# Kernel optimization log

Measured on AMD Instinct MI355X. Metric: run time of the kernel, lower is better.

## Reference

```python
import jax, jax.numpy as jnp
import numpy as np

B, S, H, NH = 4, 2048, 1024, 16
DK = H // NH


def setup_inputs() -> dict:
    key = jax.random.key(0)
    ks = jax.random.split(key, 12)
    sd = 1.0 / np.sqrt(H)
    inp = {
        "query": jax.random.normal(ks[0], (B, S, H), jnp.float32),
        "key_": jax.random.normal(ks[1], (B, S, H), jnp.float32),
        "value": jax.random.normal(ks[2], (B, S, H), jnp.float32),
        "mask": jax.random.randint(ks[3], (B, 1, S, S), 0, 2) == 1,
        "Wq": jax.random.uniform(ks[4], (H, H), jnp.float32, -sd, sd),
        "bq": jnp.zeros((H,), jnp.float32),
        "Wk": jax.random.uniform(ks[5], (H, H), jnp.float32, -sd, sd),
        "bk": jnp.zeros((H,), jnp.float32),
        "Wv": jax.random.uniform(ks[6], (H, H), jnp.float32, -sd, sd),
        "bv": jnp.zeros((H,), jnp.float32),
        "Wo": jax.random.uniform(ks[7], (H, H), jnp.float32, -sd, sd),
        "bo": jnp.zeros((H,), jnp.float32),
    }
    return inp


def reference(query, key_, value, mask, Wq, bq, Wk, bk, Wv, bv, Wo, bo):
    b = query.shape[0]
    # projections; nn.Linear computes x @ W^T + b
    q = (query @ Wq.T + bq).reshape(b, -1, NH, DK).transpose(0, 2, 1, 3)  # [B,NH,S,DK]
    k = (key_ @ Wk.T + bk).reshape(b, -1, NH, DK).transpose(0, 2, 1, 3)
    v = (value @ Wv.T + bv).reshape(b, -1, NH, DK).transpose(0, 2, 1, 3)
    scores = jnp.einsum("bhqd,bhkd->bhqk", q, k) / jnp.sqrt(jnp.float32(DK))
    min_val = jnp.finfo(scores.dtype).min
    scores = jnp.where(mask, min_val, scores)
    attn = jax.nn.softmax(scores, axis=-1)
    attn = jnp.where(mask, 0.0, attn)
    # dropout_rate = 0.0 -> identity
    x = jnp.einsum("bhqk,bhkd->bhqd", attn, v)
    x = x.transpose(0, 2, 1, 3).reshape(b, -1, NH * DK)  # [B,S,H]
    return x @ Wo.T + bo
```

## Files before the change

### kernel.cpp

```cpp
#include <hip/hip_runtime.h>
#include <hip/hip_bf16.h>
#include <stdint.h>

#define B_  4
#define S_  2048
#define H_  1024
#define NH_ 16
#define DK_ 64
#define M_  (B_*S_)

typedef unsigned short u16;
typedef __attribute__((ext_vector_type(8))) short bfrag;
typedef __attribute__((ext_vector_type(4))) float facc;
typedef __attribute__((ext_vector_type(16))) float f32x16;
typedef __attribute__((ext_vector_type(4))) unsigned int u32x4;
typedef __attribute__((ext_vector_type(2))) unsigned int u32x2;

__device__ __forceinline__ u16 f2bf(float f) {
  uint32_t u = __float_as_uint(f);
  return (u16)((u + 0x7fffu + ((u >> 16) & 1u)) >> 16);
}

__device__ __forceinline__ uint32_t cvtpk_bf16(float a, float b) {
  uint32_t r;
  asm("v_cvt_pk_bf16_f32 %0, %1, %2" : "=v"(r) : "v"(a), "v"(b));
  return r;
}

__device__ __forceinline__ f32x16 zero16() {
  f32x16 z;
  #pragma unroll
  for (int e = 0; e < 16; e++) z[e] = 0.f;
  return z;
}

__global__ void cvt3_kernel(const float* __restrict__ a0, const float* __restrict__ a1,
                            const float* __restrict__ a2,
                            u16* __restrict__ o0, u16* __restrict__ o1, u16* __restrict__ o2,
                            int n4) {
  const float* in = blockIdx.y == 0 ? a0 : blockIdx.y == 1 ? a1 : a2;
  u16* out = blockIdx.y == 0 ? o0 : blockIdx.y == 1 ? o1 : o2;
  int i = blockIdx.x * blockDim.x + threadIdx.x;
  int stride = gridDim.x * blockDim.x;
  for (; i < n4; i += stride) {
    float4 v = reinterpret_cast<const float4*>(in)[i];
    ushort4 o;
    o.x = f2bf(v.x); o.y = f2bf(v.y); o.z = f2bf(v.z); o.w = f2bf(v.w);
    reinterpret_cast<ushort4*>(out)[i] = o;
  }
}

__global__ void cvt4_kernel(const float* __restrict__ a0, const float* __restrict__ a1,
                            const float* __restrict__ a2, const float* __restrict__ a3,
                            u16* __restrict__ o0, u16* __restrict__ o1,
                            u16* __restrict__ o2, u16* __restrict__ o3,
                            int n4, float s0) {
  int y = blockIdx.y;
  const float* in = y == 0 ? a0 : y == 1 ? a1 : y == 2 ? a2 : a3;
  u16* out = y == 0 ? o0 : y == 1 ? o1 : y == 2 ? o2 : o3;
  float sc = (y == 0) ? s0 : 1.0f;
  int i = blockIdx.x * blockDim.x + threadIdx.x;
  int stride = gridDim.x * blockDim.x;
  for (; i < n4; i += stride) {
    float4 v = reinterpret_cast<const float4*>(in)[i];
    ushort4 o;
    o.x = f2bf(v.x * sc); o.y = f2bf(v.y * sc);
    o.z = f2bf(v.z * sc); o.w = f2bf(v.w * sc);
    reinterpret_cast<ushort4*>(out)[i] = o;
  }
}

__global__ void pack_mask_kernel(const int* __restrict__ m, uint32_t* __restrict__ bits, int nwords) {
  int w = blockIdx.x * blockDim.x + threadIdx.x;
  if (w >= nwords) return;
  const int4* p = reinterpret_cast<const int4*>(m) + (size_t)w * 8;
  uint32_t word = 0;
  #pragma unroll
  for (int i = 0; i < 8; i++) {
    int4 v = p[i];
    word |= (uint32_t)(v.x != 0) << (i*4);
    word |= (uint32_t)(v.y != 0) << (i*4+1);
    word |= (uint32_t)(v.z != 0) << (i*4+2);
    word |= (uint32_t)(v.w != 0) << (i*4+3);
  }
  bits[w] = word;
}

#define GLD16(gsrc, ldst) \
  __builtin_amdgcn_global_load_lds((const __attribute__((address_space(1))) void*)(gsrc), \
                                   (__attribute__((address_space(3))) void*)(ldst), 16, 0, 0)

__global__ __launch_bounds__(256) void qkv_gemm(const u16* __restrict__ qa, const u16* __restrict__ ka,
                                                const u16* __restrict__ va,
                                                const u16* __restrict__ Wqb, const u16* __restrict__ Wkb,
                                                const u16* __restrict__ Wvb,
                                                const float* __restrict__ bqp, const float* __restrict__ bkp,
                                                const float* __restrict__ bvp, float qbscale,
                                                u16* __restrict__ qh, u16* __restrict__ kh,
                                                u16* __restrict__ vt) {
  constexpr int K = H_;
  __shared__ __align__(16) u16 As[128*32];
  __shared__ __align__(16) u16 Bs[128*32];
  const int tid = threadIdx.x;
  const int lane = tid & 63, wave = tid >> 6;
  const int lo = lane & 15, hi = lane >> 4;
  const int wr = wave >> 1, wc = wave & 1;
  const int wsel = blockIdx.y >> 3;
  const int m0 = blockIdx.x * 128, n0 = (blockIdx.y & 7) * 128;
  const u16* A  = wsel == 0 ? qa : wsel == 1 ? ka : va;
  const u16* Bm = wsel == 0 ? Wqb : wsel == 1 ? Wkb : Wvb;
  const float* bias = wsel == 0 ? bqp : wsel == 1 ? bkp : bvp;
  const float bscale = wsel == 0 ? qbscale : 1.0f;
  facc acc[4][4] = {};

  for (int k0 = 0; k0 < K; k0 += 32) {
    const u16* Ab = A + (size_t)m0 * K + k0;
    const u16* Bb = Bm + (size_t)n0 * K + k0;
    #pragma unroll
    for (int i = 0; i < 2; i++) {
      int idx = i*256 + tid;
      int row = idx >> 2, q = idx & 3;
      char* la = (char*)As + i*4096 + wave*1024;
      char* lb = (char*)Bs + i*4096 + wave*1024;
      GLD16(Ab + (size_t)row*K + q*8, la);
      GLD16(Bb + (size_t)row*K + q*8, lb);
    }
    __syncthreads();
    bfrag af[4], bfv[4];
    #pragma unroll
    for (int t = 0; t < 4; t++) {
      af[t]  = *reinterpret_cast<const bfrag*>(&As[(wr*64 + t*16 + lo)*32 + hi*8]);
      bfv[t] = *reinterpret_cast<const bfrag*>(&Bs[(wc*64 + t*16 + lo)*32 + hi*8]);
    }
    #pragma unroll
    for (int mt = 0; mt < 4; mt++)
      #pragma unroll
      for (int nt = 0; nt < 4; nt++)
        acc[mt][nt] = __builtin_amdgcn_mfma_f32_16x16x32_bf16(af[mt], bfv[nt], acc[mt][nt], 0, 0, 0);
    __syncthreads();
  }

  if (wsel < 2) {
    u16* o = wsel == 0 ? qh : kh;
    #pragma unroll
    for (int nt = 0; nt < 4; nt++) {
      int n = n0 + wc*64 + nt*16 + lo;
      float bv = bias[n] * bscale;
      int hh = n >> 6, d = n & 63;
      #pragma unroll
      for (int mt = 0; mt < 4; mt++) {
        #pragma unroll
        for (int r = 0; r < 4; r++) {
          int m = m0 + wr*64 + mt*16 + hi*4 + r;
          int bb = m >> 11, s = m & (S_ - 1);
          o[(((size_t)bb*NH_ + hh)*S_ + s)*DK_ + d] = f2bf(acc[mt][nt][r] + bv);
        }
      }
    }
  } else {
    #pragma unroll
    for (int nt = 0; nt < 4; nt++) {
      int n = n0 + wc*64 + nt*16 + lo;
      float bv = bias[n];
      int hh = n >> 6, d = n & 63;
      #pragma unroll
      for (int mt = 0; mt < 4; mt++) {
        #pragma unroll
        for (int r = 0; r < 4; r++) {
          int m = m0 + wr*64 + mt*16 + hi*4 + r;
          int bb = m >> 11, s = m & (S_ - 1);
          vt[(((size_t)bb*NH_ + hh)*DK_ + d)*S_ + s] = f2bf(acc[mt][nt][r] + bv);
        }
      }
    }
  }
}

__global__ __launch_bounds__(256) void gemm_out(const u16* __restrict__ A, const u16* __restrict__ Bm,
                                                const float* __restrict__ bias, float* __restrict__ o) {
  constexpr int K = H_, N = H_;
  __shared__ __align__(16) u16 As[128*32];
  __shared__ __align__(16) u16 Bs[128*32];
  const int tid = threadIdx.x;
  const int lane = tid & 63, wave = tid >> 6;
  const int lo = lane & 15, hi = lane >> 4;
  const int wr = wave >> 1, wc = wave & 1;
  const int m0 = blockIdx.x * 128, n0 = blockIdx.y * 128;
  facc acc[4][4] = {};

  for (int k0 = 0; k0 < K; k0 += 32) {
    const u16* Ab = A + (size_t)m0 * K + k0;
    const u16* Bb = Bm + (size_t)n0 * K + k0;
    #pragma unroll
    for (int i = 0; i < 2; i++) {
      int idx = i*256 + tid;
      int row = idx >> 2, q = idx & 3;
      char* la = (char*)As + i*4096 + wave*1024;
      char* lb = (char*)Bs + i*4096 + wave*1024;
      GLD16(Ab + (size_t)row*K + q*8, la);
      GLD16(Bb + (size_t)row*K + q*8, lb);
    }
    __syncthreads();
    bfrag af[4], bfv[4];
    #pragma unroll
    for (int t = 0; t < 4; t++) {
      af[t]  = *reinterpret_cast<const bfrag*>(&As[(wr*64 + t*16 + lo)*32 + hi*8]);
      bfv[t] = *reinterpret_cast<const bfrag*>(&Bs[(wc*64 + t*16 + lo)*32 + hi*8]);
    }
    #pragma unroll
    for (int mt = 0; mt < 4; mt++)
      #pragma unroll
      for (int nt = 0; nt < 4; nt++)
        acc[mt][nt] = __builtin_amdgcn_mfma_f32_16x16x32_bf16(af[mt], bfv[nt], acc[mt][nt], 0, 0, 0);
    __syncthreads();
  }

  #pragma unroll
  for (int nt = 0; nt < 4; nt++) {
    int n = n0 + wc*64 + nt*16 + lo;
    float bv = bias[n];
    #pragma unroll
    for (int mt = 0; mt < 4; mt++) {
      #pragma unroll
      for (int r = 0; r < 4; r++) {
        int m = m0 + wr*64 + mt*16 + hi*4 + r;
        o[(size_t)m*N + n] = acc[mt][nt][r] + bv;
      }
    }
  }
}

__global__ __launch_bounds__(256, 4) void attn_kernel(const u16* __restrict__ Qh, const u16* __restrict__ Kh,
                                                      const u16* __restrict__ Vt, const uint32_t* __restrict__ mbits,
                                                      u16* __restrict__ xout) {
  __shared__ __align__(16) u16 Ks[2][64*64];
  __shared__ __align__(16) u16 Vs[2][64*64];
  const int tid = threadIdx.x;
  const int lane = tid & 63, wave = tid >> 6;
  const int l31 = lane & 31, hl = lane >> 5;
  const int gid = blockIdx.x;
  const int bh = (gid & 7) * 8 + (gid >> 7);
  const int qt = (gid >> 3) & 15;
  const int b = bh >> 4, hd = bh & 15;
  const int q0 = qt * 128;
  const size_t bhS = (size_t)bh * S_;
  const int swz = (lane & 7) << 4;

  bfrag qf[4];
  {
    const u16* qrow = Qh + (bhS + q0 + wave*32 + l31) * DK_;
    #pragma unroll
    for (int t = 0; t < 4; t++) qf[t] = *reinterpret_cast<const bfrag*>(qrow + t*16 + hl*8);
  }
  const uint32_t* mrow = mbits + ((size_t)b * S_ + q0 + wave*32 + l31) * 64;

  const int srow = wave*8 + (lane >> 3);
  const int scol = ((lane & 7) ^ (lane >> 3)) * 16;
  const char* ksrc = (const char*)(Kh + bhS * DK_) + (size_t)srow * 128 + scol;
  const char* vsrc = (const char*)(Vt + (size_t)bh * DK_ * S_) + (size_t)srow * (S_*2) + scol;

#define STAGE(buf, c) { \
    char* kl = (char*)Ks[buf] + wave*1024; \
    char* vl = (char*)Vs[buf] + wave*1024; \
    GLD16(ksrc + (size_t)(c)*8192,          kl); \
    GLD16(ksrc + (size_t)(c)*8192 + 4096,   kl + 4096); \
    GLD16(vsrc + (size_t)(c)*128,           vl); \
    GLD16(vsrc + (size_t)(c)*128 + 131072,  vl + 4096); \
  }

  float m_run = -1e29f, l_run = 0.f;
  f32x16 accO[2];
  accO[0] = zero16(); accO[1] = zero16();

  STAGE(0, 0);
  __syncthreads();

  for (int c = 0; c < 32; c++) {
    const int cur = c & 1;
    if (c + 1 < 32) STAGE(cur ^ 1, c + 1);

    const char* KsB = (const char*)Ks[cur];
    f32x16 s0 = zero16(), s1 = zero16();
    __builtin_amdgcn_s_setprio(1);
    #pragma unroll
    for (int t = 0; t < 4; t++) {
      bfrag k0 = *reinterpret_cast<const bfrag*>(KsB + l31*128        + ((t*32 + hl*16) ^ swz));
      bfrag k1 = *reinterpret_cast<const bfrag*>(KsB + (32 + l31)*128 + ((t*32 + hl*16) ^ swz));
      s0 = __builtin_amdgcn_mfma_f32_32x32x16_bf16(k0, qf[t], s0, 0, 0, 0);
      s1 = __builtin_amdgcn_mfma_f32_32x32x16_bf16(k1, qf[t], s1, 0, 0, 0);
    }
    __builtin_amdgcn_s_setprio(0);

    uint2 mwv = *reinterpret_cast<const uint2*>(mrow + c*2);
    uint32_t w0 = mwv.x >> (4*hl), w1 = mwv.y >> (4*hl);
    float sv0[16], sv1[16];
    #pragma unroll
    for (int r = 0; r < 16; r++) {
      int sh = (r & 3) + 8*(r >> 2);
      sv0[r] = ((w0 >> sh) & 1u) ? -1e30f : s0[r];
      sv1[r] = ((w1 >> sh) & 1u) ? -1e30f : s1[r];
    }
    float mc = -1e30f;
    #pragma unroll
    for (int r = 0; r < 16; r++) mc = fmaxf(mc, fmaxf(sv0[r], sv1[r]));
    mc = fmaxf(mc, __shfl_xor(mc, 32));
    if (!__all(mc <= m_run + 8.f)) {
      float mnew = fmaxf(m_run, mc);
      float alpha = __builtin_amdgcn_exp2f(m_run - mnew);
      m_run = mnew;
      l_run *= alpha;
      accO[0] = accO[0] * alpha;
      accO[1] = accO[1] * alpha;
    }
    #pragma unroll
    for (int r = 0; r < 16; r++) {
      sv0[r] = __builtin_amdgcn_exp2f(sv0[r] - m_run);
      sv1[r] = __builtin_amdgcn_exp2f(sv1[r] - m_run);
    }
    float lsum = 0.f;
    #pragma unroll
    for (int r = 0; r < 16; r++) lsum += sv0[r] + sv1[r];
    lsum += __shfl_xor(lsum, 32);
    l_run += lsum;

    u32x4 pa[4];
    #pragma unroll
    for (int kt = 0; kt < 2; kt++) {
      uint32_t W[8];
      #pragma unroll
      for (int j = 0; j < 8; j++)
        W[j] = kt == 0 ? cvtpk_bf16(sv0[2*j], sv0[2*j+1]) : cvtpk_bf16(sv1[2*j], sv1[2*j+1]);
      u32x2 r02 = __builtin_amdgcn_permlane32_swap(W[0], W[2], false, false);
      u32x2 r13 = __builtin_amdgcn_permlane32_swap(W[1], W[3], false, false);
      u32x2 r46 = __builtin_amdgcn_permlane32_swap(W[4], W[6], false, false);
      u32x2 r57 = __builtin_amdgcn_permlane32_swap(W[5], W[7], false, false);
      pa[kt*2    ][0] = r02.x; pa[kt*2    ][1] = r13.x; pa[kt*2    ][2] = r02.y; pa[kt*2    ][3] = r13.y;
      pa[kt*2 + 1][0] = r46.x; pa[kt*2 + 1][1] = r57.x; pa[kt*2 + 1][2] = r46.y; pa[kt*2 + 1][3] = r57.y;
    }

    const char* VsB = (const char*)Vs[cur];
    __builtin_amdgcn_s_setprio(1);
    #pragma unroll
    for (int ks = 0; ks < 4; ks++) {
      bfrag pb = __builtin_bit_cast(bfrag, pa[ks]);
      bfrag v0 = *reinterpret_cast<const bfrag*>(VsB + l31*128        + ((ks*32 + hl*16) ^ swz));
      bfrag v1 = *reinterpret_cast<const bfrag*>(VsB + (32 + l31)*128 + ((ks*32 + hl*16) ^ swz));
      accO[0] = __builtin_amdgcn_mfma_f32_32x32x16_bf16(v0, pb, accO[0], 0, 0, 0);
      accO[1] = __builtin_amdgcn_mfma_f32_32x32x16_bf16(v1, pb, accO[1], 0, 0, 0);
    }
    __builtin_amdgcn_s_setprio(0);
    __syncthreads();
  }
#undef STAGE

  float linv = (l_run > 0.f) ? (1.f / l_run) : 0.f;
  u16* Xs = (u16*)Ks;
  {
    char* xb = (char*)Xs + (wave*32 + l31) * 128;
    #pragma unroll
    for (int dt = 0; dt < 2; dt++)
      #pragma unroll
      for (int j = 0; j < 8; j++) {
        uint32_t w = cvtpk_bf16(accO[dt][2*j] * linv, accO[dt][2*j+1] * linv);
        int d = dt*32 + ((2*j) & 3) + 8*((2*j) >> 2) + 4*hl;
        *reinterpret_cast<uint32_t*>(xb + ((d*2) ^ swz)) = w;
      }
  }
  __syncthreads();
  {
    int row = tid >> 1, d0 = (tid & 1) * 32;
    int rsw = (row & 7) << 4;
    u16* orow = xout + ((size_t)b * S_ + q0 + row) * H_ + hd * DK_ + d0;
    #pragma unroll
    for (int i = 0; i < 4; i++) {
      bfrag v = *reinterpret_cast<const bfrag*>((char*)Xs + row*128 + ((d0*2 + i*16) ^ rsw));
      *reinterpret_cast<bfrag*>((char*)orow + i*16) = v;
    }
  }
}

extern "C" void kernel_launch(void* const* d_in, const int* in_sizes, int n_in,
                              void* d_out, int out_size, void* d_ws, size_t ws_size,
                              hipStream_t stream) {
  const float* query = (const float*)d_in[0];
  const float* key_  = (const float*)d_in[1];
  const float* value = (const float*)d_in[2];
  const int*   mask  = (const int*)d_in[3];
  const float* Wq = (const float*)d_in[4];
  const float* bq = (const float*)d_in[5];
  const float* Wk = (const float*)d_in[6];
  const float* bk = (const float*)d_in[7];
  const float* Wv = (const float*)d_in[8];
  const float* bv = (const float*)d_in[9];
  const float* Wo = (const float*)d_in[10];
  const float* bo = (const float*)d_in[11];
  float* out = (float*)d_out;

  char* ws = (char*)d_ws;
  const size_t MB = 1024 * 1024;
  u16* q_act = (u16*)(ws + 0*MB);
  u16* k_act = (u16*)(ws + 16*MB);
  u16* v_act = (u16*)(ws + 32*MB);
  u16* wq_b  = (u16*)(ws + 48*MB);
  u16* wk_b  = (u16*)(ws + 50*MB);
  u16* wv_b  = (u16*)(ws + 52*MB);
  u16* wo_b  = (u16*)(ws + 54*MB);
  u16* qh    = (u16*)(ws + 56*MB);
  u16* kh    = (u16*)(ws + 72*MB);
  u16* vt    = (u16*)(ws + 104*MB);
  u16* xb    = (u16*)(ws + 120*MB);
  uint32_t* mbits = (uint32_t*)(ws + 136*MB);

  const float QSCALE = 0.125f * 1.44269504088896f;

  const int nact4 = M_ * H_ / 4;
  cvt3_kernel<<<dim3(1024, 3), 256, 0, stream>>>(query, key_, value, q_act, k_act, v_act, nact4);
  const int nw4 = H_ * H_ / 4;
  cvt4_kernel<<<dim3(256, 4), 256, 0, stream>>>(Wq, Wk, Wv, Wo, wq_b, wk_b, wv_b, wo_b, nw4, QSCALE);
  const int nwords = B_ * S_ * S_ / 32;
  pack_mask_kernel<<<nwords/256, 256, 0, stream>>>(mask, mbits, nwords);

  qkv_gemm<<<dim3(M_/128, 24), 256, 0, stream>>>(q_act, k_act, v_act, wq_b, wk_b, wv_b,
                                                 bq, bk, bv, QSCALE, qh, kh, vt);
  attn_kernel<<<1024, 256, 0, stream>>>(qh, kh, vt, mbits, xb);
  gemm_out<<<dim3(M_/128, H_/128), 256, 0, stream>>>(xb, wo_b, bo, out);
}
```

Before: 264.4 us.

## Fold mask into MFMA accumulator init and defer row-sum shuffle to epilogue

The mask bits are now applied by seeding the QK^T MFMA accumulators with -1e30 or 0 instead of selecting after the matmul, and the mask word for the next chunk is prefetched one iteration ahead. Max and sum reductions are rewritten as balanced trees to shorten dependency chains. The cross-half shuffle for the softmax denominator moves out of the loop into the epilogue. This trims VALU work and latency in the softmax section of the attention loop. Masked scores now come from adding the dot product to -1e30, which still gives zero weight after exp.

```diff
diff --git a/kernel.cpp b/kernel.cpp
--- a/kernel.cpp
+++ b/kernel.cpp
@@ -273,14 +273,26 @@
   accO[0] = zero16(); accO[1] = zero16();
 
   STAGE(0, 0);
+  uint2 mw_cur = *reinterpret_cast<const uint2*>(mrow);
   __syncthreads();
 
   for (int c = 0; c < 32; c++) {
     const int cur = c & 1;
     if (c + 1 < 32) STAGE(cur ^ 1, c + 1);
 
+    uint2 mw = mw_cur;
+    if (c + 1 < 32) mw_cur = *reinterpret_cast<const uint2*>(mrow + (c + 1)*2);
+
+    uint32_t w0 = mw.x >> (4*hl), w1 = mw.y >> (4*hl);
+    f32x16 s0, s1;
+    #pragma unroll
+    for (int r = 0; r < 16; r++) {
+      const int sh = (r & 3) + 8*(r >> 2);
+      s0[r] = ((w0 >> sh) & 1u) ? -1e30f : 0.0f;
+      s1[r] = ((w1 >> sh) & 1u) ? -1e30f : 0.0f;
+    }
+
     const char* KsB = (const char*)Ks[cur];
-    f32x16 s0 = zero16(), s1 = zero16();
     __builtin_amdgcn_s_setprio(1);
     #pragma unroll
     for (int t = 0; t < 4; t++) {
@@ -291,18 +303,15 @@
     }
     __builtin_amdgcn_s_setprio(0);
 
-    uint2 mwv = *reinterpret_cast<const uint2*>(mrow + c*2);
-    uint32_t w0 = mwv.x >> (4*hl), w1 = mwv.y >> (4*hl);
-    float sv0[16], sv1[16];
-    #pragma unroll
-    for (int r = 0; r < 16; r++) {
-      int sh = (r & 3) + 8*(r >> 2);
-      sv0[r] = ((w0 >> sh) & 1u) ? -1e30f : s0[r];
-      sv1[r] = ((w1 >> sh) & 1u) ? -1e30f : s1[r];
-    }
-    float mc = -1e30f;
-    #pragma unroll
-    for (int r = 0; r < 16; r++) mc = fmaxf(mc, fmaxf(sv0[r], sv1[r]));
+    float t16[16];
+    #pragma unroll
+    for (int r = 0; r < 16; r++) t16[r] = fmaxf(s0[r], s1[r]);
+    float g0 = fmaxf(fmaxf(t16[0], t16[1]), t16[2]);
+    float g1 = fmaxf(fmaxf(t16[3], t16[4]), t16[5]);
+    float g2 = fmaxf(fmaxf(t16[6], t16[7]), t16[8]);
+    float g3 = fmaxf(fmaxf(t16[9], t16[10]), t16[11]);
+    float g4 = fmaxf(fmaxf(t16[12], t16[13]), t16[14]);
+    float mc = fmaxf(fmaxf(fmaxf(g0, g1), fmaxf(g2, g3)), fmaxf(g4, t16[15]));
     mc = fmaxf(mc, __shfl_xor(mc, 32));
     if (!__all(mc <= m_run + 8.f)) {
       float mnew = fmaxf(m_run, mc);
@@ -314,14 +323,13 @@
     }
     #pragma unroll
     for (int r = 0; r < 16; r++) {
-      sv0[r] = __builtin_amdgcn_exp2f(sv0[r] - m_run);
-      sv1[r] = __builtin_amdgcn_exp2f(sv1[r] - m_run);
-    }
-    float lsum = 0.f;
-    #pragma unroll
-    for (int r = 0; r < 16; r++) lsum += sv0[r] + sv1[r];
-    lsum += __shfl_xor(lsum, 32);
-    l_run += lsum;
+      s0[r] = __builtin_amdgcn_exp2f(s0[r] - m_run);
+      s1[r] = __builtin_amdgcn_exp2f(s1[r] - m_run);
+    }
+    float a8[8];
+    #pragma unroll
+    for (int r = 0; r < 8; r++) a8[r] = (s0[r] + s0[r+8]) + (s1[r] + s1[r+8]);
+    l_run += ((a8[0] + a8[1]) + (a8[2] + a8[3])) + ((a8[4] + a8[5]) + (a8[6] + a8[7]));
 
     u32x4 pa[4];
     #pragma unroll
@@ -329,13 +337,13 @@
       uint32_t W[8];
       #pragma unroll
       for (int j = 0; j < 8; j++)
-        W[j] = kt == 0 ? cvtpk_bf16(sv0[2*j], sv0[2*j+1]) : cvtpk_bf16(sv1[2*j], sv1[2*j+1]);
+        W[j] = kt == 0 ? cvtpk_bf16(s0[2*j], s0[2*j+1]) : cvtpk_bf16(s1[2*j], s1[2*j+1]);
       u32x2 r02 = __builtin_amdgcn_permlane32_swap(W[0], W[2], false, false);
       u32x2 r13 = __builtin_amdgcn_permlane32_swap(W[1], W[3], false, false);
       u32x2 r46 = __builtin_amdgcn_permlane32_swap(W[4], W[6], false, false);
       u32x2 r57 = __builtin_amdgcn_permlane32_swap(W[5], W[7], false, false);
-      pa[kt*2    ][0] = r02.x; pa[kt*2    ][1] = r13.x; pa[kt*2    ][2] = r02.y; pa[kt*2    ][3] = r13.y;
-      pa[kt*2 + 1][0] = r46.x; pa[kt*2 + 1][1] = r57.x; pa[kt*2 + 1][2] = r46.y; pa[kt*2 + 1][3] = r57.y;
+      pa[kt*2    ][0] = r02[0]; pa[kt*2    ][1] = r13[0]; pa[kt*2    ][2] = r02[1]; pa[kt*2    ][3] = r13[1];
+      pa[kt*2 + 1][0] = r46[0]; pa[kt*2 + 1][1] = r57[0]; pa[kt*2 + 1][2] = r46[1]; pa[kt*2 + 1][3] = r57[1];
     }
 
     const char* VsB = (const char*)Vs[cur];
@@ -353,7 +361,8 @@
   }
 #undef STAGE
 
-  float linv = (l_run > 0.f) ? (1.f / l_run) : 0.f;
+  float l_tot = l_run + __shfl_xor(l_run, 32);
+  float linv = (l_tot > 0.f) ? (1.f / l_tot) : 0.f;
   u16* Xs = (u16*)Ks;
   {
     char* xb = (char*)Xs + (wave*32 + l31) * 128;
```

New measurement: 259.8 us. No clear change (-1.7%).
